# Kernel optimization log

Hardware: AMD Instinct MI355X
Metric: run time of the kernel (lower is better)

## Reference

```python
import jax, jax.numpy as jnp
import numpy as np
from jax import lax

B, S, I, H, O = 128, 1024, 512, 1024, 512


def setup_inputs() -> dict:
    key = jax.random.key(0)
    ks = jax.random.split(key, 7)
    scale_ih = 1.0 / np.sqrt(H)  # torch nn.RNN init scale
    return {
        "x": jax.random.normal(ks[0], (B, S, I), dtype=jnp.float32),
        "W_ih": jax.random.uniform(ks[1], (H, I), jnp.float32, -scale_ih, scale_ih),
        "W_hh": jax.random.uniform(ks[2], (H, H), jnp.float32, -scale_ih, scale_ih),
        "b_ih": jax.random.uniform(ks[3], (H,), jnp.float32, -scale_ih, scale_ih),
        "b_hh": jax.random.uniform(ks[4], (H,), jnp.float32, -scale_ih, scale_ih),
        "W_fc": jax.random.uniform(ks[5], (O, H), jnp.float32, -scale_ih, scale_ih),
        "b_fc": jax.random.uniform(ks[6], (O,), jnp.float32, -scale_ih, scale_ih),
    }


def reference(x, W_ih, W_hh, b_ih, b_hh, W_fc, b_fc):
    # Precompute input projections for all timesteps in one big GEMM: [B,S,H]
    xp = jnp.einsum("bsi,hi->bsh", x, W_ih) + b_ih + b_hh
    h0 = jnp.zeros((x.shape[0], W_hh.shape[0]), dtype=x.dtype)

    def step(h, xt):  # h: [B,H], xt: [B,H]
        h_new = jnp.tanh(xt + h @ W_hh.T)
        return h_new, None

    hT, _ = lax.scan(step, h0, jnp.swapaxes(xp, 0, 1))  # scan over seq dim
    # fc applied to last timestep's hidden state only
    return hT @ W_fc.T + b_fc
```

## Files before the change

### kernel.cpp

```cpp
#include <hip/hip_runtime.h>
#include <stdint.h>
#include <stddef.h>
#include <math.h>

#define B_ 128
#define S_ 1024
#define I_ 512
#define H_ 1024
#define O_ 512

typedef __attribute__((ext_vector_type(4))) float f32x4;
typedef __attribute__((ext_vector_type(8))) short short8;
typedef __attribute__((ext_vector_type(2))) unsigned int uint2v;
typedef __attribute__((ext_vector_type(4))) unsigned int uint4v;

__device__ __forceinline__ unsigned short f2bf(float f) {
    unsigned u = __builtin_bit_cast(unsigned, f);
    u += 0x7fffu + ((u >> 16) & 1u);
    return (unsigned short)(u >> 16);
}
__device__ __forceinline__ uint2v pack4(f32x4 v) {
    uint2v r;
    r.x = (unsigned)f2bf(v.x) | ((unsigned)f2bf(v.y) << 16);
    r.y = (unsigned)f2bf(v.z) | ((unsigned)f2bf(v.w) << 16);
    return r;
}
__device__ __forceinline__ unsigned long long ld_u64_coh(const unsigned long long* p) {
    return __hip_atomic_load(p, __ATOMIC_RELAXED, __HIP_MEMORY_SCOPE_AGENT);
}
__device__ __forceinline__ void st_u32_coh(unsigned int* p, unsigned int v) {
    __hip_atomic_store(p, v, __ATOMIC_RELAXED, __HIP_MEMORY_SCOPE_AGENT);
}

#define OFF_WFI  2097152UL
#define OFF_HBUF 3145728UL
#define OFF_CNT  3670016UL
#define WS_NEED  (OFF_CNT + 64UL)

__global__ void rnn_init(unsigned int* hb32, unsigned int* cnt) {
    int idx = blockIdx.x * 256 + threadIdx.x;
    hb32[idx] = 0u;
    hb32[idx + 65536] = 0u;
    if (blockIdx.x == 0 && threadIdx.x < 8) cnt[threadIdx.x] = 0u;
}

__global__ void rnn_convw_hh(const float* __restrict__ Whh,
                             unsigned short* __restrict__ wfh) {
    int G = blockIdx.x * 256 + threadIdx.x;
    int l = G & 63, rest = G >> 6;
    int kc = rest & 31, t = (rest >> 5) & 1, wgn = rest >> 6;
    int n  = wgn * 32 + t * 16 + (l & 15);
    int k0 = kc * 32 + (l >> 4) * 8;
    const float* src = Whh + (size_t)n * H_ + k0;
    f32x4 f0 = *(const f32x4*)src, f1 = *(const f32x4*)(src + 4);
    uint2v a = pack4(f0), b = pack4(f1);
    uint4v pk; pk.x = a.x; pk.y = a.y; pk.z = b.x; pk.w = b.y;
    *(uint4v*)(wfh + (size_t)G * 8) = pk;
}

__global__ void rnn_convw_ih(const float* __restrict__ Wih,
                             unsigned short* __restrict__ wfi) {
    int G = blockIdx.x * 256 + threadIdx.x;
    int l = G & 63, rest = G >> 6;
    int kc2 = rest & 15, t = (rest >> 4) & 1, wgn = rest >> 5;
    int n  = wgn * 32 + t * 16 + (l & 15);
    int k0 = kc2 * 32 + (l >> 4) * 8;
    const float* src = Wih + (size_t)n * I_ + k0;
    f32x4 f0 = *(const f32x4*)src, f1 = *(const f32x4*)(src + 4);
    uint2v a = pack4(f0), b = pack4(f1);
    uint4v pk; pk.x = a.x; pk.y = a.y; pk.z = b.x; pk.w = b.y;
    *(uint4v*)(wfi + (size_t)G * 8) = pk;
}

__global__ __launch_bounds__(256, 1) void rnn_rec(
    const float* __restrict__ x,
    const unsigned short* __restrict__ wfh,
    const unsigned short* __restrict__ wfi,
    const float* __restrict__ bih, const float* __restrict__ bhh,
    unsigned short* __restrict__ hbuf,
    unsigned int* __restrict__ cnt)
{
    __shared__ unsigned short ldsH[16384];
    __shared__ unsigned short ldsX[8192];
    __shared__ float red[512];

    int g = blockIdx.x & 7, wgn = blockIdx.x >> 3;
    int tid = threadIdx.x, l = tid & 63, w = tid >> 6;
    int t = w & 1, kk = w >> 1;
    int li = l & 15, q = l >> 4;

    short8 wh[16], wi[8];
    #pragma unroll
    for (int c = 0; c < 16; ++c)
        wh[c] = *(const short8*)(wfh +
            ((size_t)((wgn * 2 + t) * 32 + kk * 16 + c)) * 512 + l * 8);
    #pragma unroll
    for (int c = 0; c < 8; ++c)
        wi[c] = *(const short8*)(wfi +
            ((size_t)((wgn * 2 + t) * 16 + kk * 8 + c)) * 512 + l * 8);

    int hcol = wgn * 32 + t * 16 + li;
    float bias = 0.f;
    if (kk == 0) bias = bih[hcol] + bhh[hcol];
    int q2 = (hcol >> 3) & 3, j2 = hcol & 7;
    unsigned int* cg = cnt + g;

    f32x4 xr[8];
    #pragma unroll
    for (int i = 0; i < 4; ++i) {
        int G = tid + i * 256, l2 = G & 63, kc2 = G >> 6;
        const float* src = x + ((size_t)(g * 16 + (l2 & 15)) * S_ + 0) * I_
                             + kc2 * 32 + (l2 >> 4) * 8;
        xr[2 * i]     = *(const f32x4*)src;
        xr[2 * i + 1] = *(const f32x4*)(src + 4);
    }
    #pragma unroll
    for (int i = 0; i < 4; ++i) {
        int G = tid + i * 256;
        uint2v a = pack4(xr[2 * i]), b = pack4(xr[2 * i + 1]);
        uint4v pk; pk.x = a.x; pk.y = a.y; pk.z = b.x; pk.w = b.y;
        *(uint4v*)&ldsX[(size_t)G * 8] = pk;
    }

    int bail = 0;
    #pragma unroll 1
    for (int s = 0; s < S_; ++s) {
        int cur = s & 1, nxt = cur ^ 1;
        const unsigned long long* hsrc = (const unsigned long long*)hbuf
            + (size_t)cur * 32768 + (size_t)g * 4096;
        unsigned long long hr[16];
        #pragma unroll
        for (int u = 0; u < 8; ++u) {
            hr[2 * u]     = ld_u64_coh(hsrc + (size_t)u * 512 + tid * 2);
            hr[2 * u + 1] = ld_u64_coh(hsrc + (size_t)u * 512 + tid * 2 + 1);
        }
        #pragma unroll
        for (int u = 0; u < 8; ++u) {
            ((unsigned long long*)ldsH)[u * 512 + tid * 2]     = hr[2 * u];
            ((unsigned long long*)ldsH)[u * 512 + tid * 2 + 1] = hr[2 * u + 1];
        }
        __syncthreads();

        f32x4 acc = {0.f, 0.f, 0.f, 0.f}, acc2 = {0.f, 0.f, 0.f, 0.f};
        #pragma unroll
        for (int c = 0; c < 16; ++c) {
            short8 a = *(const short8*)&ldsH[(kk * 16 + c) * 512 + l * 8];
            acc = __builtin_amdgcn_mfma_f32_16x16x32_bf16(a, wh[c], acc, 0, 0, 0);
        }
        #pragma unroll
        for (int c = 0; c < 8; ++c) {
            short8 a = *(const short8*)&ldsX[(kk * 8 + c) * 512 + l * 8];
            acc2 = __builtin_amdgcn_mfma_f32_16x16x32_bf16(a, wi[c], acc2, 0, 0, 0);
        }
        acc += acc2;

        int sp = (s + 1 < S_) ? s + 1 : 0;
        #pragma unroll
        for (int i = 0; i < 4; ++i) {
            int G = tid + i * 256, l2 = G & 63, kc2 = G >> 6;
            const float* src = x + ((size_t)(g * 16 + (l2 & 15)) * S_ + sp) * I_
                                 + kc2 * 32 + (l2 >> 4) * 8;
            xr[2 * i]     = *(const f32x4*)src;
            xr[2 * i + 1] = *(const f32x4*)(src + 4);
        }

        if (kk == 1) *(f32x4*)&red[t * 256 + l * 4] = acc;
        __syncthreads();
        if (kk == 0) {
            f32x4 p = *(const f32x4*)&red[t * 256 + l * 4];
            unsigned int* hout32 = (unsigned int*)(hbuf
                + (size_t)nxt * 131072 + (size_t)g * 16384
                + (size_t)wgn * 512 + j2);
            #pragma unroll
            for (int i = 0; i < 4; ++i) {
                float v = tanhf(acc[i] + p[i] + bias);
                unsigned short mybf = f2bf(v);
                unsigned nb = (unsigned)__shfl_xor((int)mybf, 1, 64) & 0xffffu;
                if ((li & 1) == 0) {
                    unsigned word = (unsigned)mybf | (nb << 16);
                    st_u32_coh(hout32 + (q2 * 16 + q * 4 + i) * 4, word);
                }
            }
        }
        #pragma unroll
        for (int i = 0; i < 4; ++i) {
            int G = tid + i * 256;
            uint2v a = pack4(xr[2 * i]), b = pack4(xr[2 * i + 1]);
            uint4v pk; pk.x = a.x; pk.y = a.y; pk.z = b.x; pk.w = b.y;
            *(uint4v*)&ldsX[(size_t)G * 8] = pk;
        }
        __syncthreads();
        if (tid == 0) {
            __hip_atomic_fetch_add(cg, 1u, __ATOMIC_RELAXED,
                                   __HIP_MEMORY_SCOPE_AGENT);
            if (!bail) {
                unsigned target = 32u * (unsigned)(s + 1);
                int polls = 0;
                while (__hip_atomic_load(cg, __ATOMIC_RELAXED,
                                         __HIP_MEMORY_SCOPE_AGENT) < target) {
                    __builtin_amdgcn_s_sleep(1);
                    if (++polls > (1 << 24)) { bail = 1; break; }
                }
            }
        }
        __syncthreads();
    }
}

__global__ __launch_bounds__(256) void rnn_fc(
    const unsigned short* __restrict__ hb0,
    const float* __restrict__ Wfc, const float* __restrict__ bfc,
    float* __restrict__ out)
{
    __shared__ unsigned short ldsB[8 * 64 * 8];
    int n_blk = blockIdx.x;
    int tid = threadIdx.x, l = tid & 63, w = tid >> 6;
    int li = l & 15, q = l >> 4;
    f32x4 acc[8][2];
    f32x4 z = {0.f, 0.f, 0.f, 0.f};
    #pragma unroll
    for (int mb = 0; mb < 8; ++mb) { acc[mb][0] = z; acc[mb][1] = z; }

    for (int kc = 0; kc < 32; ++kc) {
        #pragma unroll
        for (int u = 0; u < 2; ++u) {
            int G = tid * 2 + u;
            int nt = G >> 6, ll = G & 63;
            int n = n_blk * 128 + nt * 16 + (ll & 15);
            int k = kc * 32 + (ll >> 4) * 8;
            const float* src = Wfc + (size_t)n * H_ + k;
            f32x4 f0 = *(const f32x4*)src, f1 = *(const f32x4*)(src + 4);
            uint2v a = pack4(f0), b = pack4(f1);
            uint4v pk; pk.x = a.x; pk.y = a.y; pk.z = b.x; pk.w = b.y;
            *(uint4v*)&ldsB[G * 8] = pk;
        }
        __syncthreads();
        short8 bfr[2];
        #pragma unroll
        for (int tn = 0; tn < 2; ++tn)
            bfr[tn] = *(const short8*)&ldsB[((w * 2 + tn) * 64 + l) * 8];
        #pragma unroll
        for (int mb = 0; mb < 8; ++mb) {
            short8 a = *(const short8*)(hb0 + (size_t)mb * 16384 + kc * 512 + l * 8);
            acc[mb][0] = __builtin_amdgcn_mfma_f32_16x16x32_bf16(a, bfr[0], acc[mb][0], 0, 0, 0);
            acc[mb][1] = __builtin_amdgcn_mfma_f32_16x16x32_bf16(a, bfr[1], acc[mb][1], 0, 0, 0);
        }
        __syncthreads();
    }
    #pragma unroll
    for (int mb = 0; mb < 8; ++mb)
        #pragma unroll
        for (int tn = 0; tn < 2; ++tn)
            #pragma unroll
            for (int i = 0; i < 4; ++i) {
                int b = mb * 16 + q * 4 + i;
                int o = n_blk * 128 + (w * 2 + tn) * 16 + li;
                out[(size_t)b * O_ + o] = acc[mb][tn][i] + bfc[o];
            }
}

extern "C" void kernel_launch(void* const* d_in, const int* in_sizes, int n_in,
                              void* d_out, int out_size, void* d_ws, size_t ws_size,
                              hipStream_t stream) {
    const float* x   = (const float*)d_in[0];
    const float* Wih = (const float*)d_in[1];
    const float* Whh = (const float*)d_in[2];
    const float* bih = (const float*)d_in[3];
    const float* bhh = (const float*)d_in[4];
    const float* Wfc = (const float*)d_in[5];
    const float* bfc = (const float*)d_in[6];
    float* out = (float*)d_out;
    (void)in_sizes; (void)n_in; (void)out_size;

    if (ws_size < WS_NEED) return;

    char* ws = (char*)d_ws;
    unsigned short* wfh  = (unsigned short*)ws;
    unsigned short* wfi  = (unsigned short*)(ws + OFF_WFI);
    unsigned short* hbuf = (unsigned short*)(ws + OFF_HBUF);
    unsigned int*   cnt  = (unsigned int*)(ws + OFF_CNT);

    rnn_init<<<256, 256, 0, stream>>>((unsigned int*)hbuf, cnt);
    rnn_convw_hh<<<512, 256, 0, stream>>>(Whh, wfh);
    rnn_convw_ih<<<256, 256, 0, stream>>>(Wih, wfi);

    const float* xa = x; const float* biha = bih; const float* bhha = bhh;
    void* args[] = {(void*)&xa, (void*)&wfh, (void*)&wfi,
                    (void*)&biha, (void*)&bhha, (void*)&hbuf, (void*)&cnt};
    hipLaunchCooperativeKernel((const void*)rnn_rec, dim3(256), dim3(256),
                               args, 0, stream);

    rnn_fc<<<4, 256, 0, stream>>>(hbuf, Wfc, bfc, out);
}
```

Baseline: 5.631 ms.

## Replace atomic-counter barrier with per-block flags and load h directly into registers

```diff
diff --git a/kernel.cpp b/kernel.cpp
--- a/kernel.cpp
+++ b/kernel.cpp
@@ -31,17 +31,20 @@
 __device__ __forceinline__ void st_u32_coh(unsigned int* p, unsigned int v) {
     __hip_atomic_store(p, v, __ATOMIC_RELAXED, __HIP_MEMORY_SCOPE_AGENT);
 }
+__device__ __forceinline__ unsigned int ld_u32_coh(const unsigned int* p) {
+    return __hip_atomic_load(p, __ATOMIC_RELAXED, __HIP_MEMORY_SCOPE_AGENT);
+}
 
 #define OFF_WFI  2097152UL
 #define OFF_HBUF 3145728UL
 #define OFF_CNT  3670016UL
-#define WS_NEED  (OFF_CNT + 64UL)
+#define WS_NEED  (OFF_CNT + 2048UL)
 
 __global__ void rnn_init(unsigned int* hb32, unsigned int* cnt) {
     int idx = blockIdx.x * 256 + threadIdx.x;
     hb32[idx] = 0u;
     hb32[idx + 65536] = 0u;
-    if (blockIdx.x == 0 && threadIdx.x < 8) cnt[threadIdx.x] = 0u;
+    if (blockIdx.x < 2) cnt[blockIdx.x * 256 + threadIdx.x] = 0u;
 }
 
 __global__ void rnn_convw_hh(const float* __restrict__ Whh,
@@ -80,7 +83,6 @@
     unsigned short* __restrict__ hbuf,
     unsigned int* __restrict__ cnt)
 {
-    __shared__ unsigned short ldsH[16384];
     __shared__ unsigned short ldsX[8192];
     __shared__ float red[512];
 
@@ -103,66 +105,70 @@
     float bias = 0.f;
     if (kk == 0) bias = bih[hcol] + bhh[hcol];
     int q2 = (hcol >> 3) & 3, j2 = hcol & 7;
-    unsigned int* cg = cnt + g;
-
-    f32x4 xr[8];
-    #pragma unroll
-    for (int i = 0; i < 4; ++i) {
-        int G = tid + i * 256, l2 = G & 63, kc2 = G >> 6;
-        const float* src = x + ((size_t)(g * 16 + (l2 & 15)) * S_ + 0) * I_
-                             + kc2 * 32 + (l2 >> 4) * 8;
-        xr[2 * i]     = *(const f32x4*)src;
-        xr[2 * i + 1] = *(const f32x4*)(src + 4);
+    unsigned int* flg = cnt + g * 64;
+
+    {
+        f32x4 xr[8];
+        #pragma unroll
+        for (int i = 0; i < 4; ++i) {
+            int G = tid + i * 256, l2 = G & 63, kc2 = G >> 6;
+            const float* src = x + ((size_t)(g * 16 + (l2 & 15)) * S_ + 0) * I_
+                                 + kc2 * 32 + (l2 >> 4) * 8;
+            xr[2 * i]     = *(const f32x4*)src;
+            xr[2 * i + 1] = *(const f32x4*)(src + 4);
+        }
+        #pragma unroll
+        for (int i = 0; i < 4; ++i) {
+            int G = tid + i * 256;
+            uint2v a = pack4(xr[2 * i]), b = pack4(xr[2 * i + 1]);
+            uint4v pk; pk.x = a.x; pk.y = a.y; pk.z = b.x; pk.w = b.y;
+            *(uint4v*)&ldsX[(size_t)G * 8] = pk;
+        }
     }
-    #pragma unroll
-    for (int i = 0; i < 4; ++i) {
-        int G = tid + i * 256;
-        uint2v a = pack4(xr[2 * i]), b = pack4(xr[2 * i + 1]);
-        uint4v pk; pk.x = a.x; pk.y = a.y; pk.z = b.x; pk.w = b.y;
-        *(uint4v*)&ldsX[(size_t)G * 8] = pk;
-    }
+    __syncthreads();
 
     int bail = 0;
     #pragma unroll 1
     for (int s = 0; s < S_; ++s) {
         int cur = s & 1, nxt = cur ^ 1;
+        int havex = (s + 1 < S_);
+
         const unsigned long long* hsrc = (const unsigned long long*)hbuf
-            + (size_t)cur * 32768 + (size_t)g * 4096;
-        unsigned long long hr[16];
-        #pragma unroll
-        for (int u = 0; u < 8; ++u) {
-            hr[2 * u]     = ld_u64_coh(hsrc + (size_t)u * 512 + tid * 2);
-            hr[2 * u + 1] = ld_u64_coh(hsrc + (size_t)u * 512 + tid * 2 + 1);
-        }
-        #pragma unroll
-        for (int u = 0; u < 8; ++u) {
-            ((unsigned long long*)ldsH)[u * 512 + tid * 2]     = hr[2 * u];
-            ((unsigned long long*)ldsH)[u * 512 + tid * 2 + 1] = hr[2 * u + 1];
-        }
-        __syncthreads();
-
-        f32x4 acc = {0.f, 0.f, 0.f, 0.f}, acc2 = {0.f, 0.f, 0.f, 0.f};
+            + (size_t)cur * 32768 + (size_t)g * 4096
+            + (size_t)kk * 2048 + (size_t)l * 2;
+        unsigned long long h0[16], h1[16];
         #pragma unroll
         for (int c = 0; c < 16; ++c) {
-            short8 a = *(const short8*)&ldsH[(kk * 16 + c) * 512 + l * 8];
-            acc = __builtin_amdgcn_mfma_f32_16x16x32_bf16(a, wh[c], acc, 0, 0, 0);
-        }
+            h0[c] = ld_u64_coh(hsrc + (size_t)c * 128);
+            h1[c] = ld_u64_coh(hsrc + (size_t)c * 128 + 1);
+        }
+
+        f32x4 xr[8];
+        if (havex) {
+            #pragma unroll
+            for (int i = 0; i < 4; ++i) {
+                int G = tid + i * 256, l2 = G & 63, kc2 = G >> 6;
+                const float* src = x + ((size_t)(g * 16 + (l2 & 15)) * S_ + (s + 1)) * I_
+                                     + kc2 * 32 + (l2 >> 4) * 8;
+                xr[2 * i]     = *(const f32x4*)src;
+                xr[2 * i + 1] = *(const f32x4*)(src + 4);
+            }
+        }
+
+        f32x4 acc2 = {0.f, 0.f, 0.f, 0.f};
         #pragma unroll
         for (int c = 0; c < 8; ++c) {
             short8 a = *(const short8*)&ldsX[(kk * 8 + c) * 512 + l * 8];
             acc2 = __builtin_amdgcn_mfma_f32_16x16x32_bf16(a, wi[c], acc2, 0, 0, 0);
         }
+        f32x4 acc = {0.f, 0.f, 0.f, 0.f};
+        #pragma unroll
+        for (int c = 0; c < 16; ++c) {
+            union { unsigned long long qw[2]; short8 v; } u;
+            u.qw[0] = h0[c]; u.qw[1] = h1[c];
+            acc = __builtin_amdgcn_mfma_f32_16x16x32_bf16(u.v, wh[c], acc, 0, 0, 0);
+        }
         acc += acc2;
-
-        int sp = (s + 1 < S_) ? s + 1 : 0;
-        #pragma unroll
-        for (int i = 0; i < 4; ++i) {
-            int G = tid + i * 256, l2 = G & 63, kc2 = G >> 6;
-            const float* src = x + ((size_t)(g * 16 + (l2 & 15)) * S_ + sp) * I_
-                                 + kc2 * 32 + (l2 >> 4) * 8;
-            xr[2 * i]     = *(const f32x4*)src;
-            xr[2 * i + 1] = *(const f32x4*)(src + 4);
-        }
 
         if (kk == 1) *(f32x4*)&red[t * 256 + l * 4] = acc;
         __syncthreads();
@@ -182,28 +188,29 @@
                 }
             }
         }
-        #pragma unroll
-        for (int i = 0; i < 4; ++i) {
-            int G = tid + i * 256;
-            uint2v a = pack4(xr[2 * i]), b = pack4(xr[2 * i + 1]);
-            uint4v pk; pk.x = a.x; pk.y = a.y; pk.z = b.x; pk.w = b.y;
-            *(uint4v*)&ldsX[(size_t)G * 8] = pk;
-        }
         __syncthreads();
-        if (tid == 0) {
-            __hip_atomic_fetch_add(cg, 1u, __ATOMIC_RELAXED,
-                                   __HIP_MEMORY_SCOPE_AGENT);
-            if (!bail) {
-                unsigned target = 32u * (unsigned)(s + 1);
+
+        if (havex) {
+            if (tid == 0) st_u32_coh(flg + wgn, (unsigned)(s + 1));
+            #pragma unroll
+            for (int i = 0; i < 4; ++i) {
+                int G = tid + i * 256;
+                uint2v a = pack4(xr[2 * i]), b2 = pack4(xr[2 * i + 1]);
+                uint4v pk; pk.x = a.x; pk.y = a.y; pk.z = b2.x; pk.w = b2.y;
+                *(uint4v*)&ldsX[(size_t)G * 8] = pk;
+            }
+            if (tid < 64 && !bail) {
+                unsigned target = (unsigned)(s + 1);
                 int polls = 0;
-                while (__hip_atomic_load(cg, __ATOMIC_RELAXED,
-                                         __HIP_MEMORY_SCOPE_AGENT) < target) {
+                while (true) {
+                    unsigned v = ld_u32_coh(flg + (l & 31));
+                    if (__ballot((int)(v >= target)) == ~0ull) break;
                     __builtin_amdgcn_s_sleep(1);
-                    if (++polls > (1 << 24)) { bail = 1; break; }
+                    if (++polls > (1 << 22)) { bail = 1; break; }
                 }
             }
-        }
-        __syncthreads();
+            __syncthreads();
+        }
     }
 }
 
```

Measured after the change: 4.800 ms. 1.17x faster.
